# Kernel optimization log

Measured on AMD Instinct MI355X. Metric: run time of the kernel, lower is better.

Reference implementation:

```python
import jax, jax.numpy as jnp
import numpy as np
from math import ceil

B, T, FQ, D = 2, 48, 100, 512
H, DFF, L, WSZ = 8, 2048, 6, 8


def setup_inputs() -> dict:
    key = jax.random.key(0)
    ks = jax.random.split(key, 8)
    g = lambda k, shape: jax.random.normal(k, shape, jnp.float32) * 0.02
    return {
        "frame_queries": jax.random.normal(ks[0], (B, T, FQ, D), jnp.float32),
        "Wp": g(ks[1], (D, D)), "bp": jnp.zeros((D,), jnp.float32),
        "Wqkv": g(ks[2], (L, 3 * D, D)), "bqkv": jnp.zeros((L, 3 * D), jnp.float32),
        "Wo": g(ks[3], (L, D, D)), "bo": jnp.zeros((L, D), jnp.float32),
        "ln1_s": jnp.ones((L, D), jnp.float32), "ln1_b": jnp.zeros((L, D), jnp.float32),
        "W1": g(ks[4], (L, DFF, D)), "b1": jnp.zeros((L, DFF), jnp.float32),
        "W2": g(ks[5], (L, D, DFF)), "b2": jnp.zeros((L, D), jnp.float32),
        "ln2_s": jnp.ones((L, D), jnp.float32), "ln2_b": jnp.zeros((L, D), jnp.float32),
    }


def _ln(x, s, b, eps=1e-5):
    mu = x.mean(-1, keepdims=True)
    var = ((x - mu) ** 2).mean(-1, keepdims=True)
    return (x - mu) * jax.lax.rsqrt(var + eps) * s + b


def _mha(x, Wqkv_i, bqkv_i, Wo_i, bo_i, add_mask):
    # x: [Bw, S, C]; add_mask: None or [Bw, 1, S, S] additive float
    Bw, S, C = x.shape
    hd = C // H
    qkv = x @ Wqkv_i.T + bqkv_i
    q, k, v = jnp.split(qkv, 3, axis=-1)
    q = q.reshape(Bw, S, H, hd).transpose(0, 2, 1, 3)
    k = k.reshape(Bw, S, H, hd).transpose(0, 2, 1, 3)
    v = v.reshape(Bw, S, H, hd).transpose(0, 2, 1, 3)
    scores = jnp.einsum('bhqd,bhkd->bhqk', q, k) * jnp.float32(1.0 / np.sqrt(hd))
    if add_mask is not None:
        scores = scores + add_mask
    a = jax.nn.softmax(scores, axis=-1)
    o = jnp.einsum('bhqk,bhkd->bhqd', a, v).transpose(0, 2, 1, 3).reshape(Bw, S, C)
    return o @ Wo_i.T + bo_i


def _shift_mask():
    # padding mask is all-False (T % WSZ == 0), faithful construction of the
    # shifted-window additive mask as in the torch code.
    Nw = T // WSZ
    half = int(ceil(WSZ / 2))
    S = WSZ * FQ
    am = jnp.zeros((B, T), dtype=bool)
    r = jnp.roll(am, half, axis=1).reshape(B, Nw, WSZ)
    m = jnp.broadcast_to(r[..., None], (B, Nw, WSZ, WSZ))
    m = m.at[:, 0].set(m[:, 0] | m[:, 0].swapaxes(-1, -2))
    m = m.at[:, -1].set(m[:, -1] | m[:, -1].swapaxes(-1, -2))
    m = m.at[:, 0, :half, half:].set(True)
    m = m.at[:, 0, half:, :half].set(True)
    mfull = jnp.broadcast_to(m.reshape(B * Nw, WSZ, 1, WSZ, 1),
                             (B * Nw, WSZ, FQ, WSZ, FQ)).reshape(B * Nw, S, S)
    return (mfull.astype(jnp.float32) * -1000.0)[:, None]  # [B*Nw,1,S,S]


def reference(frame_queries, Wp, bp, Wqkv, bqkv, Wo, bo, ln1_s, ln1_b,
              W1, b1, W2, b2, ln2_s, ln2_b):
    Nw = T // WSZ
    half = int(ceil(WSZ / 2))
    S = WSZ * FQ
    x = frame_queries @ Wp.T + bp  # [B, T, FQ, D]
    shift_add = _shift_mask()
    for i in range(L):
        if i % 2 == 0:
            # plain window attention
            xw = x.reshape(B * Nw, S, D)
            xw = _ln(xw + _mha(xw, Wqkv[i], bqkv[i], Wo[i], bo[i], None),
                     ln1_s[i], ln1_b[i])
            x = xw.reshape(B, T, FQ, D)
        else:
            # shifted window attention
            xs = jnp.roll(x, half, axis=1)
            xw = xs.reshape(B * Nw, S, D)
            xw = _ln(xw + _mha(xw, Wqkv[i], bqkv[i], Wo[i], bo[i], shift_add),
                     ln1_s[i], ln1_b[i])
            x = jnp.roll(xw.reshape(B, T, FQ, D), -half, axis=1)
        # FFN (pointwise over channel dim)
        h = jax.nn.relu(x @ W1[i].T + b1[i]) @ W2[i].T + b2[i]
        x = _ln(x + h, ln2_s[i], ln2_b[i])
    return x  # [B, T, FQ, D] == 'lb t nq c'
```

## Files before the change

kernel.cpp:

```cpp
#include <hip/hip_runtime.h>


typedef float  f4    __attribute__((ext_vector_type(4)));
typedef __bf16 bf8   __attribute__((ext_vector_type(8)));
typedef unsigned short u16x8 __attribute__((ext_vector_type(8)));
typedef unsigned short u16x4 __attribute__((ext_vector_type(4)));

__device__ __forceinline__ unsigned short f2bf(float f) {
    unsigned int u = __builtin_bit_cast(unsigned int, f);
    u += 0x7fffu + ((u >> 16) & 1u);
    return (unsigned short)(u >> 16);
}
__device__ __forceinline__ float bf2f(unsigned short s) {
    return __builtin_bit_cast(float, ((unsigned int)s) << 16);
}

#define GLD16(gp, lp) __builtin_amdgcn_global_load_lds( \
    (const __attribute__((address_space(1))) void*)(gp), \
    (__attribute__((address_space(3))) void*)(lp), 16, 0, 0)

__device__ __forceinline__ int map_row(int r, int rshift) {
    if (!rshift) return r;
    int bb = r / 4800, rem = r % 4800;
    int tt = rem / 100, f = rem - tt * 100;
    return bb * 4800 + ((tt + rshift) % 48) * 100 + f;
}

template<int BM>
__global__ __launch_bounds__(256) void mfma_gemm(
    const unsigned short* __restrict__ A, const unsigned short* __restrict__ W,
    const float* __restrict__ bias, float* Cf, unsigned short* Cb,
    int M, int N, int K, int relu, int rshift, int qscale)
{
    constexpr int MI      = BM / 32;
    constexpr int ABUF    = BM * 64;
    constexpr int AROUNDS = BM / 32;
    __shared__ unsigned short As[2 * ABUF];
    __shared__ unsigned short Bs[2 * 8192];
    const int tid = threadIdx.x, lane = tid & 63, wave = tid >> 6;
    const int n0 = blockIdx.x * 128, m0 = blockIdx.y * BM;

    const unsigned short* ga[AROUNDS];
    unsigned short* la[AROUNDS];
    #pragma unroll
    for (int it = 0; it < AROUNDS; ++it) {
        int s = it * 256 + tid, row = s >> 3, cg = (s & 7) ^ (row & 7);
        ga[it] = A + (size_t)map_row(m0 + row, rshift) * K + cg * 8;
        la[it] = &As[(it * 256 + wave * 64) * 8];
    }
    const unsigned short* gb[4];
    unsigned short* lb[4];
    #pragma unroll
    for (int it = 0; it < 4; ++it) {
        int s = it * 256 + tid, row = s >> 3, cg = (s & 7) ^ (row & 7);
        gb[it] = W + (size_t)(n0 + row) * K + cg * 8;
        lb[it] = &Bs[(it * 256 + wave * 64) * 8];
    }

    const int wm = (wave >> 1) * (BM / 2), wn = (wave & 1) * 64;
    const int lr = lane & 15, quad = lane >> 4;

    f4 acc[MI][4];
    #pragma unroll
    for (int i = 0; i < MI; ++i)
        #pragma unroll
        for (int j = 0; j < 4; ++j) acc[i][j] = 0.f;

    #pragma unroll
    for (int it = 0; it < AROUNDS; ++it) GLD16(ga[it], la[it]);
    #pragma unroll
    for (int it = 0; it < 4; ++it) GLD16(gb[it], lb[it]);

    const int NK = K >> 6;
    for (int kt = 0; kt < NK; ++kt) {
        const int cb = kt & 1, nb = cb ^ 1;
        __syncthreads();
        if (kt + 1 < NK) {
            const int k1 = (kt + 1) << 6;
            #pragma unroll
            for (int it = 0; it < AROUNDS; ++it) GLD16(ga[it] + k1, la[it] + nb * ABUF);
            #pragma unroll
            for (int it = 0; it < 4; ++it)       GLD16(gb[it] + k1, lb[it] + nb * 8192);
        }
        const unsigned short* Ab = &As[cb * ABUF];
        const unsigned short* Bb = &Bs[cb * 8192];
        #pragma unroll
        for (int kh = 0; kh < 2; ++kh) {
            bf8 af[MI], bfr[4];
            #pragma unroll
            for (int mi = 0; mi < MI; ++mi) {
                int m = wm + mi * 16 + lr;
                int c = (kh * 4 + quad) ^ (m & 7);
                af[mi] = __builtin_bit_cast(bf8, *(const u16x8*)&Ab[(m * 8 + c) * 8]);
            }
            #pragma unroll
            for (int ni = 0; ni < 4; ++ni) {
                int n = wn + ni * 16 + lr;
                int c = (kh * 4 + quad) ^ (n & 7);
                bfr[ni] = __builtin_bit_cast(bf8, *(const u16x8*)&Bb[(n * 8 + c) * 8]);
            }
            #pragma unroll
            for (int mi = 0; mi < MI; ++mi)
                #pragma unroll
                for (int ni = 0; ni < 4; ++ni)
                    acc[mi][ni] = __builtin_amdgcn_mfma_f32_16x16x32_bf16(
                        af[mi], bfr[ni], acc[mi][ni], 0, 0, 0);
        }
    }

    #pragma unroll
    for (int mi = 0; mi < MI; ++mi) {
        #pragma unroll
        for (int ni = 0; ni < 4; ++ni) {
            const int rowg = m0 + wm + mi * 16 + quad * 4;
            const int colg = n0 + wn + ni * 16 + lr;
            const float bv = bias[colg];
            const float sc = (qscale && colg < 512) ? 0.125f : 1.0f;
            #pragma unroll
            for (int r = 0; r < 4; ++r) {
                float v = (acc[mi][ni][r] + bv) * sc;
                if (relu) v = fmaxf(v, 0.f);
                const size_t off = (size_t)(rowg + r) * N + colg;
                if (Cf) Cf[off] = v;
                if (Cb) Cb[off] = f2bf(v);
            }
        }
    }
}

__global__ __launch_bounds__(320) void flash_attn_mfma(
    const unsigned short* __restrict__ qkv, unsigned short* __restrict__ o,
    int masked)
{
    __shared__ unsigned short Ks[2][2048];
    __shared__ unsigned short VT[2][64 * 34];
    __shared__ unsigned short Ps[5][2][576];

    const int qt = blockIdx.x, h = blockIdx.y, w = blockIdx.z;
    const int tid = threadIdx.x, lane = tid & 63, wave = tid >> 6;
    const int lr = lane & 15, quad = lane >> 4;
    const int qb = qt * 160 + wave * 16;
    const int qw[2] = { qb, qb + 80 };
    const size_t wbase = (size_t)w * 800 * 1536;
    const bool do_mask = masked && ((w % 6) == 0);

    bf8 aQ[2][2];
    #pragma unroll
    for (int s2 = 0; s2 < 2; ++s2) {
        const unsigned short* qp =
            qkv + wbase + (size_t)(qw[s2] + lr) * 1536 + h * 64 + quad * 8;
        aQ[s2][0] = __builtin_bit_cast(bf8, *(const u16x8*)qp);
        aQ[s2][1] = __builtin_bit_cast(bf8, *(const u16x8*)(qp + 32));
    }

    const unsigned short* gk = qkv;
    int kw = 0;
    if (wave < 4) {
        int s = wave * 64 + lane, row = s >> 3, clog = (s & 7) ^ (row & 7);
        gk = qkv + wbase + (size_t)row * 1536 + 512 + h * 64 + clog * 8;
        kw = wave * 512;
    }
    const int vkey = tid >> 3, vd0 = (tid & 7) * 8;
    const unsigned short* gv =
        qkv + wbase + (size_t)vkey * 1536 + 1024 + h * 64 + vd0;

    float lsum[2] = {0.f, 0.f};
    f4 oacc[2][4];
    #pragma unroll
    for (int s2 = 0; s2 < 2; ++s2)
        #pragma unroll
        for (int dt = 0; dt < 4; ++dt) oacc[s2][dt] = 0.f;

    bool qhl[2];
    #pragma unroll
    for (int s2 = 0; s2 < 2; ++s2) qhl[s2] = (qw[s2] + lr) >= 400;

    if (wave < 4) GLD16(gk, &Ks[0][kw]);
    if (tid < 256) {
        u16x8 vv0 = *(const u16x8*)gv;
        #pragma unroll
        for (int j = 0; j < 8; ++j) VT[0][(vd0 + j) * 34 + vkey] = vv0[j];
    }

    for (int kt = 0; kt < 25; ++kt) {
        const int cb = kt & 1, nb = cb ^ 1;
        const int k0 = kt * 32;
        __syncthreads();

        u16x8 vv;
        const bool pf = (kt < 24);
        if (pf && wave < 4) GLD16(gk + (size_t)(k0 + 32) * 1536, &Ks[nb][kw]);
        if (pf && tid < 256) vv = *(const u16x8*)(gv + (size_t)(k0 + 32) * 1536);

        f4 st[2][2];
        st[0][0] = 0.f; st[0][1] = 0.f; st[1][0] = 0.f; st[1][1] = 0.f;
        #pragma unroll
        for (int kh = 0; kh < 2; ++kh) {
            const int cx = (kh * 4 + quad) ^ (lane & 7);
            bf8 kf0 = __builtin_bit_cast(bf8, *(const u16x8*)&Ks[cb][(lr * 8 + cx) * 8]);
            bf8 kf1 = __builtin_bit_cast(bf8, *(const u16x8*)&Ks[cb][((16 + lr) * 8 + cx) * 8]);
            st[0][0] = __builtin_amdgcn_mfma_f32_16x16x32_bf16(kf0, aQ[0][kh], st[0][0], 0, 0, 0);
            st[0][1] = __builtin_amdgcn_mfma_f32_16x16x32_bf16(kf1, aQ[0][kh], st[0][1], 0, 0, 0);
            st[1][0] = __builtin_amdgcn_mfma_f32_16x16x32_bf16(kf0, aQ[1][kh], st[1][0], 0, 0, 0);
            st[1][1] = __builtin_amdgcn_mfma_f32_16x16x32_bf16(kf1, aQ[1][kh], st[1][1], 0, 0, 0);
        }

        #pragma unroll
        for (int s2 = 0; s2 < 2; ++s2) {
            u16x4 pk0, pk1;
            float ls = 0.f;
            #pragma unroll
            for (int r = 0; r < 4; ++r) {
                float a = st[s2][0][r], b = st[s2][1][r];
                if (do_mask) {
                    if (((k0 + quad * 4 + r) >= 400) != qhl[s2])      a -= 1000.f;
                    if (((k0 + 16 + quad * 4 + r) >= 400) != qhl[s2]) b -= 1000.f;
                }
                float p0 = __expf(fminf(a, 80.f));
                float p1 = __expf(fminf(b, 80.f));
                ls += p0 + p1;
                pk0[r] = (unsigned short)(__builtin_bit_cast(unsigned int, p0) >> 16);
                pk1[r] = (unsigned short)(__builtin_bit_cast(unsigned int, p1) >> 16);
            }
            lsum[s2] += ls;
            *(u16x4*)&Ps[wave][s2][lr * 36 + quad * 4]      = pk0;
            *(u16x4*)&Ps[wave][s2][lr * 36 + 16 + quad * 4] = pk1;
        }

        if (pf && tid < 256) {
            #pragma unroll
            for (int j = 0; j < 8; ++j) VT[nb][(vd0 + j) * 34 + vkey] = vv[j];
        }

        bf8 aP0 = __builtin_bit_cast(bf8, *(const u16x8*)&Ps[wave][0][lr * 36 + quad * 8]);
        bf8 aP1 = __builtin_bit_cast(bf8, *(const u16x8*)&Ps[wave][1][lr * 36 + quad * 8]);
        #pragma unroll
        for (int dt = 0; dt < 4; ++dt) {
            bf8 bV = __builtin_bit_cast(bf8,
                *(const u16x8*)&VT[cb][(dt * 16 + lr) * 34 + quad * 8]);
            oacc[0][dt] = __builtin_amdgcn_mfma_f32_16x16x32_bf16(aP0, bV, oacc[0][dt], 0, 0, 0);
            oacc[1][dt] = __builtin_amdgcn_mfma_f32_16x16x32_bf16(aP1, bV, oacc[1][dt], 0, 0, 0);
        }
    }

    #pragma unroll
    for (int s2 = 0; s2 < 2; ++s2) {
        float l = lsum[s2];
        l += __shfl_xor(l, 16);
        l += __shfl_xor(l, 32);
        float inv[4];
        #pragma unroll
        for (int r = 0; r < 4; ++r)
            inv[r] = 1.0f / __shfl(l, quad * 4 + r);
        #pragma unroll
        for (int dt = 0; dt < 4; ++dt)
            #pragma unroll
            for (int r = 0; r < 4; ++r)
                o[((size_t)w * 800 + qw[s2] + quad * 4 + r) * 512 + h * 64 + dt * 16 + lr] =
                    f2bf(oacc[s2][dt][r] * inv[r]);
    }
}

__global__ __launch_bounds__(256) void add_ln_kernel(
    const unsigned short* xb, const unsigned short* dlt,
    const float* __restrict__ s, const float* __restrict__ b,
    float* outf, unsigned short* outb, int rshift)
{
    const int wave = threadIdx.x >> 6, lane = threadIdx.x & 63;
    const int row = blockIdx.x * 4 + wave;
    const int xrow = map_row(row, rshift);
    const int c = lane * 8;
    u16x8 xv = *(const u16x8*)(xb  + (size_t)xrow * 512 + c);
    u16x8 dv = *(const u16x8*)(dlt + (size_t)row  * 512 + c);
    f4 u0, u1;
    #pragma unroll
    for (int j = 0; j < 4; ++j) {
        u0[j] = bf2f(xv[j])     + bf2f(dv[j]);
        u1[j] = bf2f(xv[4 + j]) + bf2f(dv[4 + j]);
    }
    float sum = u0[0]+u0[1]+u0[2]+u0[3] + u1[0]+u1[1]+u1[2]+u1[3];
    #pragma unroll
    for (int o2 = 1; o2 < 64; o2 <<= 1) sum += __shfl_xor(sum, o2);
    const float mu = sum * (1.0f / 512.0f);
    f4 d0 = u0 - mu, d1 = u1 - mu;
    float sq = d0[0]*d0[0]+d0[1]*d0[1]+d0[2]*d0[2]+d0[3]*d0[3]
             + d1[0]*d1[0]+d1[1]*d1[1]+d1[2]*d1[2]+d1[3]*d1[3];
    #pragma unroll
    for (int o2 = 1; o2 < 64; o2 <<= 1) sq += __shfl_xor(sq, o2);
    const float rs = rsqrtf(sq * (1.0f / 512.0f) + 1e-5f);
    f4 s0 = *(const f4*)(s + c), s1 = *(const f4*)(s + c + 4);
    f4 b0 = *(const f4*)(b + c), b1 = *(const f4*)(b + c + 4);
    f4 y0, y1;
    #pragma unroll
    for (int j = 0; j < 4; ++j) { y0[j] = d0[j]*rs*s0[j]+b0[j]; y1[j] = d1[j]*rs*s1[j]+b1[j]; }
    u16x8 ob;
    #pragma unroll
    for (int j = 0; j < 4; ++j) { ob[j] = f2bf(y0[j]); ob[4+j] = f2bf(y1[j]); }
    *(u16x8*)(outb + (size_t)xrow * 512 + c) = ob;
    if (outf) {
        float* of = outf + (size_t)xrow * 512 + c;
        *(f4*)of = y0; *(f4*)(of + 4) = y1;
    }
}

__global__ __launch_bounds__(256) void cast_f2b_kernel(
    const float* __restrict__ in, unsigned short* __restrict__ out, int n4)
{
    const int i = blockIdx.x * 256 + threadIdx.x;
    if (i >= n4) return;
    f4 v = ((const f4*)in)[i];
    u16x4 o4 = {f2bf(v[0]), f2bf(v[1]), f2bf(v[2]), f2bf(v[3])};
    ((u16x4*)out)[i] = o4;
}

extern "C" void kernel_launch(void* const* d_in, const int* in_sizes, int n_in,
                              void* d_out, int out_size, void* d_ws, size_t ws_size,
                              hipStream_t stream)
{
    const float* fq   = (const float*)d_in[0];
    const float* Wp   = (const float*)d_in[1];
    const float* bp   = (const float*)d_in[2];
    const float* Wqkv = (const float*)d_in[3];
    const float* bqkv = (const float*)d_in[4];
    const float* Wo   = (const float*)d_in[5];
    const float* bo   = (const float*)d_in[6];
    const float* l1s  = (const float*)d_in[7];
    const float* l1b  = (const float*)d_in[8];
    const float* W1   = (const float*)d_in[9];
    const float* b1   = (const float*)d_in[10];
    const float* W2   = (const float*)d_in[11];
    const float* b2   = (const float*)d_in[12];
    const float* l2s  = (const float*)d_in[13];
    const float* l2b  = (const float*)d_in[14];
    float* out = (float*)d_out;

    unsigned short* xb   = (unsigned short*)d_ws;
    unsigned short* qkvb = xb + 4915200;
    unsigned short* hbuf = qkvb + 14745600;
    unsigned short* wbuf = hbuf + 19660800;
    unsigned short* obuf = hbuf;
    unsigned short* t1b  = qkvb;
    unsigned short* fqb  = hbuf;
    unsigned short* wqA = wbuf;
    unsigned short* woA = wqA + 4718592;
    unsigned short* w1A = woA + 1572864;
    unsigned short* w2A = w1A + 6291456;
    unsigned short* wpA = w2A + 6291456;

    const dim3 blk(256);
    cast_f2b_kernel<<<dim3(4800), blk, 0, stream>>>(fq,   fqb, 1228800);
    cast_f2b_kernel<<<dim3(4608), blk, 0, stream>>>(Wqkv, wqA, 1179648);
    cast_f2b_kernel<<<dim3(1536), blk, 0, stream>>>(Wo,   woA, 393216);
    cast_f2b_kernel<<<dim3(6144), blk, 0, stream>>>(W1,   w1A, 1572864);
    cast_f2b_kernel<<<dim3(6144), blk, 0, stream>>>(W2,   w2A, 1572864);
    cast_f2b_kernel<<<dim3(256),  blk, 0, stream>>>(Wp,   wpA, 65536);
    mfma_gemm<64><<<dim3(4, 150), blk, 0, stream>>>(fqb, wpA, bp, nullptr, xb,
                                                    9600, 512, 512, 0, 0, 0);

    for (int i = 0; i < 6; ++i) {
        const int rsh = (i & 1) ? 44 : 0;
        const unsigned short* wq = wqA + (size_t)i * 786432;
        const unsigned short* wo = woA + (size_t)i * 262144;
        const unsigned short* w1 = w1A + (size_t)i * 1048576;
        const unsigned short* w2 = w2A + (size_t)i * 1048576;
        mfma_gemm<128><<<dim3(12, 75), blk, 0, stream>>>(xb, wq, bqkv + i * 1536,
                                                         nullptr, qkvb, 9600, 1536, 512, 0, rsh, 1);
        flash_attn_mfma<<<dim3(5, 8, 12), dim3(320), 0, stream>>>(qkvb, obuf, i & 1);
        mfma_gemm<64><<<dim3(4, 150), blk, 0, stream>>>(obuf, wo, bo + i * 512,
                                                        nullptr, t1b, 9600, 512, 512, 0, 0, 0);
        add_ln_kernel<<<dim3(2400), blk, 0, stream>>>(xb, t1b, l1s + i * 512, l1b + i * 512,
                                                      nullptr, xb, rsh);
        mfma_gemm<128><<<dim3(16, 75), blk, 0, stream>>>(xb, w1, b1 + i * 2048,
                                                         nullptr, hbuf, 9600, 2048, 512, 1, 0, 0);
        mfma_gemm<64><<<dim3(4, 150), blk, 0, stream>>>(hbuf, w2, b2 + i * 512,
                                                        nullptr, t1b, 9600, 512, 2048, 0, 0, 0);
        add_ln_kernel<<<dim3(2400), blk, 0, stream>>>(xb, t1b, l2s + i * 512, l2b + i * 512,
                                                      (i == 5) ? out : nullptr, xb, 0);
    }
}
```

Before: 1.207 ms.

## Halve GEMM K-tile to 32 and split attention query tiles for more blocks

The GEMM now stages 32-wide K slices instead of 64, halving LDS use per block and changing the swizzle to match. This should let more blocks fit per CU, at the cost of twice as many K iterations and barriers. The attention kernel now gives each wave one 16-row query tile instead of two and launches 960 blocks on a flat grid with head-fastest ordering. That raises parallelism and lowers register pressure, but K/V tiles are reloaded by twice as many blocks.

```diff
diff --git a/kernel.cpp b/kernel.cpp
--- a/kernel.cpp
+++ b/kernel.cpp
@@ -33,10 +33,10 @@
     int M, int N, int K, int relu, int rshift, int qscale)
 {
     constexpr int MI      = BM / 32;
-    constexpr int ABUF    = BM * 64;
-    constexpr int AROUNDS = BM / 32;
+    constexpr int ABUF    = BM * 32;
+    constexpr int AROUNDS = BM / 64;
     __shared__ unsigned short As[2 * ABUF];
-    __shared__ unsigned short Bs[2 * 8192];
+    __shared__ unsigned short Bs[2 * 4096];
     const int tid = threadIdx.x, lane = tid & 63, wave = tid >> 6;
     const int n0 = blockIdx.x * 128, m0 = blockIdx.y * BM;
 
@@ -44,15 +44,15 @@
     unsigned short* la[AROUNDS];
     #pragma unroll
     for (int it = 0; it < AROUNDS; ++it) {
-        int s = it * 256 + tid, row = s >> 3, cg = (s & 7) ^ (row & 7);
+        int s = it * 256 + tid, row = s >> 2, cg = (s & 3) ^ ((row >> 1) & 3);
         ga[it] = A + (size_t)map_row(m0 + row, rshift) * K + cg * 8;
         la[it] = &As[(it * 256 + wave * 64) * 8];
     }
-    const unsigned short* gb[4];
-    unsigned short* lb[4];
-    #pragma unroll
-    for (int it = 0; it < 4; ++it) {
-        int s = it * 256 + tid, row = s >> 3, cg = (s & 7) ^ (row & 7);
+    const unsigned short* gb[2];
+    unsigned short* lb[2];
+    #pragma unroll
+    for (int it = 0; it < 2; ++it) {
+        int s = it * 256 + tid, row = s >> 2, cg = (s & 3) ^ ((row >> 1) & 3);
         gb[it] = W + (size_t)(n0 + row) * K + cg * 8;
         lb[it] = &Bs[(it * 256 + wave * 64) * 8];
     }
@@ -69,43 +69,41 @@
     #pragma unroll
     for (int it = 0; it < AROUNDS; ++it) GLD16(ga[it], la[it]);
     #pragma unroll
-    for (int it = 0; it < 4; ++it) GLD16(gb[it], lb[it]);
-
-    const int NK = K >> 6;
+    for (int it = 0; it < 2; ++it) GLD16(gb[it], lb[it]);
+
+    const int NK = K >> 5;
     for (int kt = 0; kt < NK; ++kt) {
         const int cb = kt & 1, nb = cb ^ 1;
         __syncthreads();
         if (kt + 1 < NK) {
-            const int k1 = (kt + 1) << 6;
+            const int k1 = (kt + 1) << 5;
             #pragma unroll
             for (int it = 0; it < AROUNDS; ++it) GLD16(ga[it] + k1, la[it] + nb * ABUF);
             #pragma unroll
-            for (int it = 0; it < 4; ++it)       GLD16(gb[it] + k1, lb[it] + nb * 8192);
+            for (int it = 0; it < 2; ++it)       GLD16(gb[it] + k1, lb[it] + nb * 4096);
         }
         const unsigned short* Ab = &As[cb * ABUF];
-        const unsigned short* Bb = &Bs[cb * 8192];
-        #pragma unroll
-        for (int kh = 0; kh < 2; ++kh) {
-            bf8 af[MI], bfr[4];
-            #pragma unroll
-            for (int mi = 0; mi < MI; ++mi) {
-                int m = wm + mi * 16 + lr;
-                int c = (kh * 4 + quad) ^ (m & 7);
-                af[mi] = __builtin_bit_cast(bf8, *(const u16x8*)&Ab[(m * 8 + c) * 8]);
-            }
-            #pragma unroll
-            for (int ni = 0; ni < 4; ++ni) {
-                int n = wn + ni * 16 + lr;
-                int c = (kh * 4 + quad) ^ (n & 7);
-                bfr[ni] = __builtin_bit_cast(bf8, *(const u16x8*)&Bb[(n * 8 + c) * 8]);
-            }
-            #pragma unroll
-            for (int mi = 0; mi < MI; ++mi)
-                #pragma unroll
-                for (int ni = 0; ni < 4; ++ni)
-                    acc[mi][ni] = __builtin_amdgcn_mfma_f32_16x16x32_bf16(
-                        af[mi], bfr[ni], acc[mi][ni], 0, 0, 0);
-        }
+        const unsigned short* Bb = &Bs[cb * 4096];
+        bf8 af[MI], bfr[4];
+        #pragma unroll
+        for (int mi = 0; mi < MI; ++mi) {
+            int m = wm + mi * 16 + lr;
+            int c = quad ^ ((m >> 1) & 3);
+            af[mi] = __builtin_bit_cast(bf8, *(const u16x8*)&Ab[(m * 4 + c) * 8]);
+        }
+        #pragma unroll
+        for (int ni = 0; ni < 4; ++ni) {
+            int n = wn + ni * 16 + lr;
+            int c = quad ^ ((n >> 1) & 3);
+            bfr[ni] = __builtin_bit_cast(bf8, *(const u16x8*)&Bs[cb * 4096 + (n * 4 + c) * 8]);
+        }
+        #pragma unroll
+        for (int mi = 0; mi < MI; ++mi)
+            #pragma unroll
+            for (int ni = 0; ni < 4; ++ni)
+                acc[mi][ni] = __builtin_amdgcn_mfma_f32_16x16x32_bf16(
+                    af[mi], bfr[ni], acc[mi][ni], 0, 0, 0);
+        (void)Ab;
     }
 
     #pragma unroll
@@ -134,23 +132,23 @@
 {
     __shared__ unsigned short Ks[2][2048];
     __shared__ unsigned short VT[2][64 * 34];
-    __shared__ unsigned short Ps[5][2][576];
-
-    const int qt = blockIdx.x, h = blockIdx.y, w = blockIdx.z;
+    __shared__ unsigned short Ps[5][576];
+
+    const int bid = blockIdx.x;
+    const int h = bid & 7, kk2 = bid >> 3;
+    const int qt = kk2 % 10, w = kk2 / 10;
     const int tid = threadIdx.x, lane = tid & 63, wave = tid >> 6;
     const int lr = lane & 15, quad = lane >> 4;
-    const int qb = qt * 160 + wave * 16;
-    const int qw[2] = { qb, qb + 80 };
+    const int qb = qt * 80 + wave * 16;
     const size_t wbase = (size_t)w * 800 * 1536;
     const bool do_mask = masked && ((w % 6) == 0);
 
-    bf8 aQ[2][2];
-    #pragma unroll
-    for (int s2 = 0; s2 < 2; ++s2) {
+    bf8 aQ[2];
+    {
         const unsigned short* qp =
-            qkv + wbase + (size_t)(qw[s2] + lr) * 1536 + h * 64 + quad * 8;
-        aQ[s2][0] = __builtin_bit_cast(bf8, *(const u16x8*)qp);
-        aQ[s2][1] = __builtin_bit_cast(bf8, *(const u16x8*)(qp + 32));
+            qkv + wbase + (size_t)(qb + lr) * 1536 + h * 64 + quad * 8;
+        aQ[0] = __builtin_bit_cast(bf8, *(const u16x8*)qp);
+        aQ[1] = __builtin_bit_cast(bf8, *(const u16x8*)(qp + 32));
     }
 
     const unsigned short* gk = qkv;
@@ -164,16 +162,12 @@
     const unsigned short* gv =
         qkv + wbase + (size_t)vkey * 1536 + 1024 + h * 64 + vd0;
 
-    float lsum[2] = {0.f, 0.f};
-    f4 oacc[2][4];
-    #pragma unroll
-    for (int s2 = 0; s2 < 2; ++s2)
-        #pragma unroll
-        for (int dt = 0; dt < 4; ++dt) oacc[s2][dt] = 0.f;
-
-    bool qhl[2];
-    #pragma unroll
-    for (int s2 = 0; s2 < 2; ++s2) qhl[s2] = (qw[s2] + lr) >= 400;
+    float lsum = 0.f;
+    f4 oacc[4];
+    #pragma unroll
+    for (int dt = 0; dt < 4; ++dt) oacc[dt] = 0.f;
+
+    const bool qhl = (qb + lr) >= 400;
 
     if (wave < 4) GLD16(gk, &Ks[0][kw]);
     if (tid < 256) {
@@ -192,29 +186,26 @@
         if (pf && wave < 4) GLD16(gk + (size_t)(k0 + 32) * 1536, &Ks[nb][kw]);
         if (pf && tid < 256) vv = *(const u16x8*)(gv + (size_t)(k0 + 32) * 1536);
 
-        f4 st[2][2];
-        st[0][0] = 0.f; st[0][1] = 0.f; st[1][0] = 0.f; st[1][1] = 0.f;
+        f4 st[2];
+        st[0] = 0.f; st[1] = 0.f;
         #pragma unroll
         for (int kh = 0; kh < 2; ++kh) {
             const int cx = (kh * 4 + quad) ^ (lane & 7);
             bf8 kf0 = __builtin_bit_cast(bf8, *(const u16x8*)&Ks[cb][(lr * 8 + cx) * 8]);
             bf8 kf1 = __builtin_bit_cast(bf8, *(const u16x8*)&Ks[cb][((16 + lr) * 8 + cx) * 8]);
-            st[0][0] = __builtin_amdgcn_mfma_f32_16x16x32_bf16(kf0, aQ[0][kh], st[0][0], 0, 0, 0);
-            st[0][1] = __builtin_amdgcn_mfma_f32_16x16x32_bf16(kf1, aQ[0][kh], st[0][1], 0, 0, 0);
-            st[1][0] = __builtin_amdgcn_mfma_f32_16x16x32_bf16(kf0, aQ[1][kh], st[1][0], 0, 0, 0);
-            st[1][1] = __builtin_amdgcn_mfma_f32_16x16x32_bf16(kf1, aQ[1][kh], st[1][1], 0, 0, 0);
-        }
-
-        #pragma unroll
-        for (int s2 = 0; s2 < 2; ++s2) {
+            st[0] = __builtin_amdgcn_mfma_f32_16x16x32_bf16(kf0, aQ[kh], st[0], 0, 0, 0);
+            st[1] = __builtin_amdgcn_mfma_f32_16x16x32_bf16(kf1, aQ[kh], st[1], 0, 0, 0);
+        }
+
+        {
             u16x4 pk0, pk1;
             float ls = 0.f;
             #pragma unroll
             for (int r = 0; r < 4; ++r) {
-                float a = st[s2][0][r], b = st[s2][1][r];
+                float a = st[0][r], b = st[1][r];
                 if (do_mask) {
-                    if (((k0 + quad * 4 + r) >= 400) != qhl[s2])      a -= 1000.f;
-                    if (((k0 + 16 + quad * 4 + r) >= 400) != qhl[s2]) b -= 1000.f;
+                    if (((k0 + quad * 4 + r) >= 400) != qhl)      a -= 1000.f;
+                    if (((k0 + 16 + quad * 4 + r) >= 400) != qhl) b -= 1000.f;
                 }
                 float p0 = __expf(fminf(a, 80.f));
                 float p1 = __expf(fminf(b, 80.f));
@@ -222,9 +213,9 @@
                 pk0[r] = (unsigned short)(__builtin_bit_cast(unsigned int, p0) >> 16);
                 pk1[r] = (unsigned short)(__builtin_bit_cast(unsigned int, p1) >> 16);
             }
-            lsum[s2] += ls;
-            *(u16x4*)&Ps[wave][s2][lr * 36 + quad * 4]      = pk0;
-            *(u16x4*)&Ps[wave][s2][lr * 36 + 16 + quad * 4] = pk1;
+            lsum += ls;
+            *(u16x4*)&Ps[wave][lr * 36 + quad * 4]      = pk0;
+            *(u16x4*)&Ps[wave][lr * 36 + 16 + quad * 4] = pk1;
         }
 
         if (pf && tid < 256) {
@@ -232,20 +223,17 @@
             for (int j = 0; j < 8; ++j) VT[nb][(vd0 + j) * 34 + vkey] = vv[j];
         }
 
-        bf8 aP0 = __builtin_bit_cast(bf8, *(const u16x8*)&Ps[wave][0][lr * 36 + quad * 8]);
-        bf8 aP1 = __builtin_bit_cast(bf8, *(const u16x8*)&Ps[wave][1][lr * 36 + quad * 8]);
+        bf8 aP = __builtin_bit_cast(bf8, *(const u16x8*)&Ps[wave][lr * 36 + quad * 8]);
         #pragma unroll
         for (int dt = 0; dt < 4; ++dt) {
             bf8 bV = __builtin_bit_cast(bf8,
                 *(const u16x8*)&VT[cb][(dt * 16 + lr) * 34 + quad * 8]);
-            oacc[0][dt] = __builtin_amdgcn_mfma_f32_16x16x32_bf16(aP0, bV, oacc[0][dt], 0, 0, 0);
-            oacc[1][dt] = __builtin_amdgcn_mfma_f32_16x16x32_bf16(aP1, bV, oacc[1][dt], 0, 0, 0);
-        }
-    }
-
-    #pragma unroll
-    for (int s2 = 0; s2 < 2; ++s2) {
-        float l = lsum[s2];
+            oacc[dt] = __builtin_amdgcn_mfma_f32_16x16x32_bf16(aP, bV, oacc[dt], 0, 0, 0);
+        }
+    }
+
+    {
+        float l = lsum;
         l += __shfl_xor(l, 16);
         l += __shfl_xor(l, 32);
         float inv[4];
@@ -256,8 +244,8 @@
         for (int dt = 0; dt < 4; ++dt)
             #pragma unroll
             for (int r = 0; r < 4; ++r)
-                o[((size_t)w * 800 + qw[s2] + quad * 4 + r) * 512 + h * 64 + dt * 16 + lr] =
-                    f2bf(oacc[s2][dt][r] * inv[r]);
+                o[((size_t)w * 800 + qb + quad * 4 + r) * 512 + h * 64 + dt * 16 + lr] =
+                    f2bf(oacc[dt][r] * inv[r]);
     }
 }
 
@@ -365,7 +353,7 @@
         const unsigned short* w2 = w2A + (size_t)i * 1048576;
         mfma_gemm<128><<<dim3(12, 75), blk, 0, stream>>>(xb, wq, bqkv + i * 1536,
                                                          nullptr, qkvb, 9600, 1536, 512, 0, rsh, 1);
-        flash_attn_mfma<<<dim3(5, 8, 12), dim3(320), 0, stream>>>(qkvb, obuf, i & 1);
+        flash_attn_mfma<<<dim3(960), dim3(320), 0, stream>>>(qkvb, obuf, i & 1);
         mfma_gemm<64><<<dim3(4, 150), blk, 0, stream>>>(obuf, wo, bo + i * 512,
                                                         nullptr, t1b, 9600, 512, 512, 0, 0, 0);
         add_ln_kernel<<<dim3(2400), blk, 0, stream>>>(xb, t1b, l1s + i * 512, l1b + i * 512,
```

New measurement: 1.248 ms. +3.3%, slower.
